# Kernel optimization log

Hardware: AMD Instinct MI355X
Metric: run time of the kernel (lower is better)

The kernel has to match this reference:

```python
import jax, jax.numpy as jnp
import numpy as np

B, L, E, C = 256, 1024, 128, 5  # trees, leaves per tree, embed size, num classes

def setup_inputs() -> dict:
    key = jax.random.key(0)
    k1, k2, k3 = jax.random.split(key, 3)
    leaves = jax.random.normal(k1, (B, L, E), dtype=jnp.float32)
    # Glorot-ish scaling so 10 stacked relu(Linear) levels stay well-conditioned
    W = jax.random.normal(k2, (E, 2 * E), dtype=jnp.float32) * (2.0 / (2 * E)) ** 0.5
    bW = jnp.zeros((E,), dtype=jnp.float32)
    P = jax.random.normal(k3, (C, E), dtype=jnp.float32) * (2.0 / E) ** 0.5
    bP = jnp.zeros((C,), dtype=jnp.float32)
    return {"leaves": leaves, "W": W, "bW": bW, "P": P, "bP": bP}

def reference(leaves, W, bW, P, bP):
    """Batched level-by-level bottom-up pass over a forest of perfect binary trees.
    Per internal node (same math as RecursiveNN.traverse):
        h = relu(W @ concat(left, right) + bW)
        proj = P @ h + bP
    Returns all internal-node projections concatenated: [B*(L-1), C].
    """
    x = leaves  # [B, n, E] current frontier of node embeddings
    probs = []
    while x.shape[1] > 1:
        # pair adjacent siblings: [B, n/2, 2E]
        pairs = jnp.concatenate([x[:, 0::2], x[:, 1::2]], axis=-1)
        h = jax.nn.relu(jnp.einsum('bnf,ef->bne', pairs, W) + bW)  # [B, n/2, E]
        proj = jnp.einsum('bne,ce->bnc', h, P) + bP                # [B, n/2, C]
        probs.append(proj.reshape(-1, P.shape[0]))
        x = h
    return jnp.concatenate(probs, axis=0)  # [B*(L-1), C]
```

## Files before the change

kernel.cpp:

```cpp
#include <hip/hip_runtime.h>
#include <hip/hip_bf16.h>
#include <hip/hip_fp16.h>


typedef _Float16 f16_t;
typedef _Float16 f16x4 __attribute__((ext_vector_type(4)));
typedef _Float16 f16x8 __attribute__((ext_vector_type(8)));
typedef float f32x4 __attribute__((ext_vector_type(4)));

#define HSTRIDE 136

static __device__ __forceinline__ f32x4 mfma16(f16x8 a, f16x8 b, f32x4 c) {
    return __builtin_amdgcn_mfma_f32_16x16x32_f16(a, b, c, 0, 0, 0);
}

static __device__ __forceinline__ f16x8 cvt8(const float* p) {
    const float4 a = *(const float4*)p;
    const float4 b = *(const float4*)(p + 4);
    f16x8 t = { (f16_t)a.x, (f16_t)a.y, (f16_t)a.z, (f16_t)a.w,
                (f16_t)b.x, (f16_t)b.y, (f16_t)b.z, (f16_t)b.w };
    return t;
}

__global__ __launch_bounds__(256, 2)
void forest_kernel(const float* __restrict__ leaves,
                   const float* __restrict__ W,
                   const float* __restrict__ P,
                   const float* __restrict__ bW,
                   const float* __restrict__ bP,
                   f16_t* __restrict__ Q,
                   float* __restrict__ out)
{
    __shared__ f16_t Stg[2][32 * HSTRIDE];
    __shared__ f16_t Hbuf[64 * HSTRIDE];

    const int tid   = threadIdx.x;
    const int wave  = tid >> 6;
    const int lane  = tid & 63;
    const int mlane = lane & 15;
    const int q     = lane >> 4;
    const int tree  = blockIdx.x >> 3;
    const int e     = blockIdx.x & 7;
    const size_t m0 = (size_t)blockIdx.x * 64;
    const float* leafbase = leaves + (size_t)blockIdx.x * 16384;

    auto store_stage = [&](int buf, const float4* pf) {
        #pragma unroll
        for (int r = 0; r < 4; ++r) {
            const int idx = tid + r * 256;
            const int row = idx >> 5;
            const int c4  = idx & 31;
            f16x4 t4 = { (f16_t)pf[r].x, (f16_t)pf[r].y, (f16_t)pf[r].z, (f16_t)pf[r].w };
            *(f16x4*)&Stg[buf][row * HSTRIDE + c4 * 4] = t4;
        }
    };

    float4 pf[4];
    #pragma unroll
    for (int r = 0; r < 4; ++r) pf[r] = ((const float4*)leafbase)[tid + r * 256];

    f16x8 wh[2][8];
    float bwv[2];
    #pragma unroll
    for (int n = 0; n < 2; ++n) {
        const int col = wave * 32 + n * 16 + mlane;
        bwv[n] = bW[col];
        #pragma unroll
        for (int k = 0; k < 8; ++k)
            wh[n][k] = cvt8(&W[col * 256 + k * 32 + q * 8]);
    }

    f16x8 pb[4] = {};
    if (mlane < 5) {
        #pragma unroll
        for (int kb = 0; kb < 4; ++kb)
            pb[kb] = cvt8(&P[mlane * 128 + kb * 32 + q * 8]);
    }
    const float bpv = (mlane < 5) ? bP[mlane] : 0.f;

    store_stage(0, pf);

    auto proj_store = [&](int hrow0, size_t orow0, int valid) {
        f32x4 pc = {};
        #pragma unroll
        for (int kb = 0; kb < 4; ++kb) {
            const f16x8 ha = *(const f16x8*)&Hbuf[(hrow0 + mlane) * HSTRIDE + kb * 32 + q * 8];
            pc = mfma16(ha, pb[kb], pc);
        }
        if (mlane < 5) {
            #pragma unroll
            for (int r = 0; r < 4; ++r) {
                const int row = q * 4 + r;
                if (row < valid) out[(orow0 + row) * 5 + mlane] = pc[r] + bpv;
            }
        }
    };

    for (int c = 0; c < 4; ++c) {
        __syncthreads();
        if (c < 3) {
            #pragma unroll
            for (int r = 0; r < 4; ++r)
                pf[r] = ((const float4*)leafbase)[(c + 1) * 1024 + tid + r * 256];
        }
        f16x8 af[8];
        const f16_t* sb = Stg[c & 1];
        #pragma unroll
        for (int k = 0; k < 8; ++k) {
            const int off  = k * 64 + q * 16;
            const int trow = off >> 8;
            const int ce   = (off & 255) >> 1;
            af[k] = *(const f16x8*)&sb[(2 * mlane + trow) * HSTRIDE + ce];
        }
        f32x4 acc0 = {}, acc1 = {};
        #pragma unroll
        for (int k = 0; k < 8; ++k) {
            acc0 = mfma16(af[k], wh[0][k], acc0);
            acc1 = mfma16(af[k], wh[1][k], acc1);
        }
        if (c < 3) store_stage((c + 1) & 1, pf);

        #pragma unroll
        for (int r = 0; r < 4; ++r) {
            float v0 = fmaxf(acc0[r] + bwv[0], 0.f);
            float v1 = fmaxf(acc1[r] + bwv[1], 0.f);
            Hbuf[(c * 16 + q * 4 + r) * HSTRIDE + wave * 32 + mlane]      = (f16_t)v0;
            Hbuf[(c * 16 + q * 4 + r) * HSTRIDE + wave * 32 + 16 + mlane] = (f16_t)v1;
        }
        __syncthreads();

        if (wave == 0) proj_store(c * 16, m0 + c * 16, 16);
    }

    int Mprev = 64;
    #pragma unroll 1
    for (int j = 2; j <= 7; ++j) {
        const int Mnew   = Mprev >> 1;
        const int chunks = (Mnew + 15) >> 4;
        const size_t off_j = 256 * (1024 - (2048 >> j));
        const size_t base_j = off_j + (size_t)tree * (1024 >> j) + (size_t)e * (128 >> j);
        for (int c = 0; c < chunks; ++c) {
            f16x8 af[8];
            #pragma unroll
            for (int k = 0; k < 8; ++k) {
                const int off  = k * 64 + q * 16;
                const int trow = off >> 8;
                const int ce   = (off & 255) >> 1;
                af[k] = *(const f16x8*)&Hbuf[(32 * c + 2 * mlane + trow) * HSTRIDE + ce];
            }
            __syncthreads();
            f32x4 acc0 = {}, acc1 = {};
            #pragma unroll
            for (int k = 0; k < 8; ++k) {
                acc0 = mfma16(af[k], wh[0][k], acc0);
                acc1 = mfma16(af[k], wh[1][k], acc1);
            }
            #pragma unroll
            for (int r = 0; r < 4; ++r) {
                float v0 = fmaxf(acc0[r] + bwv[0], 0.f);
                float v1 = fmaxf(acc1[r] + bwv[1], 0.f);
                Hbuf[(c * 16 + q * 4 + r) * HSTRIDE + wave * 32 + mlane]      = (f16_t)v0;
                Hbuf[(c * 16 + q * 4 + r) * HSTRIDE + wave * 32 + 16 + mlane] = (f16_t)v1;
            }
            __syncthreads();

            const int valid = (Mnew - c * 16 < 16) ? (Mnew - c * 16) : 16;
            if (wave == 0)
                proj_store(c * 16, base_j + c * 16, valid);
        }
        Mprev = Mnew;
    }

    if (tid < 16)
        *(uint4*)&Q[(size_t)blockIdx.x * 128 + tid * 8] = *(const uint4*)&Hbuf[tid * 8];
}

__global__ __launch_bounds__(128, 4)
void rnn_top_kernel(const f16_t* __restrict__ Q,
                    const float* __restrict__ W,
                    const float* __restrict__ bW,
                    const float* __restrict__ P,
                    const float* __restrict__ bP,
                    float* __restrict__ out)
{
    __shared__ float qs[1024];
    __shared__ float hs[896];
    const int t    = threadIdx.x;
    const int tree = blockIdx.x;

    #pragma unroll
    for (int i = 0; i < 8; ++i)
        qs[t + i * 128] = (float)Q[(size_t)tree * 1024 + t + i * 128];
    __syncthreads();

    const float* wr = W + t * 256;

    float s8[4];
    #pragma unroll
    for (int n = 0; n < 4; ++n) s8[n] = bW[t];
    for (int k = 0; k < 256; k += 4) {
        const float4 wv = *(const float4*)(wr + k);
        #pragma unroll
        for (int n = 0; n < 4; ++n) {
            const float* qb = qs + n * 256 + k;
            s8[n] += wv.x * qb[0] + wv.y * qb[1] + wv.z * qb[2] + wv.w * qb[3];
        }
    }
    #pragma unroll
    for (int n = 0; n < 4; ++n) hs[n * 128 + t] = fmaxf(s8[n], 0.f);
    __syncthreads();

    float s9[2];
    s9[0] = s9[1] = bW[t];
    for (int k = 0; k < 256; k += 4) {
        const float4 wv = *(const float4*)(wr + k);
        #pragma unroll
        for (int m = 0; m < 2; ++m) {
            const float* hb = hs + m * 256 + k;
            s9[m] += wv.x * hb[0] + wv.y * hb[1] + wv.z * hb[2] + wv.w * hb[3];
        }
    }
    hs[512 + t] = fmaxf(s9[0], 0.f);
    hs[640 + t] = fmaxf(s9[1], 0.f);
    __syncthreads();

    float s10 = bW[t];
    for (int k = 0; k < 256; k += 4) {
        const float4 wv = *(const float4*)(wr + k);
        const float* hb = hs + 512 + k;
        s10 += wv.x * hb[0] + wv.y * hb[1] + wv.z * hb[2] + wv.w * hb[3];
    }
    hs[768 + t] = fmaxf(s10, 0.f);
    __syncthreads();

    if (t < 35) {
        const int node = t / 5, c = t % 5;
        float s = bP[c];
        const float* hb = hs + node * 128;
        for (int k = 0; k < 128; ++k) s += hb[k] * P[c * 128 + k];
        size_t row;
        if (node < 4)      row = 260096 + (size_t)tree * 4 + node;
        else if (node < 6) row = 261120 + (size_t)tree * 2 + (node - 4);
        else               row = 261632 + (size_t)tree;
        out[row * 5 + c] = s;
    }
}

extern "C" void kernel_launch(void* const* d_in, const int* in_sizes, int n_in,
                              void* d_out, int out_size, void* d_ws, size_t ws_size,
                              hipStream_t stream) {
    const float* leaves = (const float*)d_in[0];
    const float* W      = (const float*)d_in[1];
    const float* bW     = (const float*)d_in[2];
    const float* P      = (const float*)d_in[3];
    const float* bP     = (const float*)d_in[4];
    float* out = (float*)d_out;

    f16_t* Q = (f16_t*)d_ws;

    forest_kernel<<<dim3(2048), dim3(256), 0, stream>>>(leaves, W, P, bW, bP, Q, out);
    rnn_top_kernel<<<dim3(256), dim3(128), 0, stream>>>(Q, W, bW, P, bP, out);
}
```

Baseline: 248.0 us.

## Preconvert weights to fp16, bulk-load leaves, and stage upper-level outputs in LDS

A new prep kernel converts W and P to fp16 once, so each forest block loads half-precision weights directly instead of converting fp32 on every block. The double-buffered leaf pipeline is replaced by one bulk load of all 64 leaf rows into a larger LDS arena. The level-1 projection is now spread across all four waves after a single barrier. Projections for levels 2-7 are buffered in shared memory and written out cooperatively at the end, rather than as scattered small stores from a single wave. In exchange there is an extra kernel launch and more LDS per block, which may reduce occupancy, and the load/compute overlap of the old pipeline is lost.

```diff
diff --git a/kernel.cpp b/kernel.cpp
--- a/kernel.cpp
+++ b/kernel.cpp
@@ -14,25 +14,28 @@
     return __builtin_amdgcn_mfma_f32_16x16x32_f16(a, b, c, 0, 0, 0);
 }
 
-static __device__ __forceinline__ f16x8 cvt8(const float* p) {
-    const float4 a = *(const float4*)p;
-    const float4 b = *(const float4*)(p + 4);
-    f16x8 t = { (f16_t)a.x, (f16_t)a.y, (f16_t)a.z, (f16_t)a.w,
-                (f16_t)b.x, (f16_t)b.y, (f16_t)b.z, (f16_t)b.w };
-    return t;
+__global__ void prep_kernel(const float* __restrict__ W, const float* __restrict__ P,
+                            f16_t* __restrict__ Wh, f16_t* __restrict__ Ph) {
+    if (blockIdx.x < 128) {
+        const int i = blockIdx.x * 256 + threadIdx.x;
+        Wh[i] = (f16_t)W[i];
+    } else {
+        for (int i = threadIdx.x; i < 640; i += 256) Ph[i] = (f16_t)P[i];
+    }
 }
 
 __global__ __launch_bounds__(256, 2)
 void forest_kernel(const float* __restrict__ leaves,
-                   const float* __restrict__ W,
-                   const float* __restrict__ P,
+                   const f16_t* __restrict__ Wh,
+                   const f16_t* __restrict__ Ph,
                    const float* __restrict__ bW,
                    const float* __restrict__ bP,
                    f16_t* __restrict__ Q,
                    float* __restrict__ out)
 {
-    __shared__ f16_t Stg[2][32 * HSTRIDE];
+    __shared__ f16_t Arena[128 * HSTRIDE];
     __shared__ f16_t Hbuf[64 * HSTRIDE];
+    __shared__ float OutB[320];
 
     const int tid   = threadIdx.x;
     const int wave  = tid >> 6;
@@ -44,21 +47,6 @@
     const size_t m0 = (size_t)blockIdx.x * 64;
     const float* leafbase = leaves + (size_t)blockIdx.x * 16384;
 
-    auto store_stage = [&](int buf, const float4* pf) {
-        #pragma unroll
-        for (int r = 0; r < 4; ++r) {
-            const int idx = tid + r * 256;
-            const int row = idx >> 5;
-            const int c4  = idx & 31;
-            f16x4 t4 = { (f16_t)pf[r].x, (f16_t)pf[r].y, (f16_t)pf[r].z, (f16_t)pf[r].w };
-            *(f16x4*)&Stg[buf][row * HSTRIDE + c4 * 4] = t4;
-        }
-    };
-
-    float4 pf[4];
-    #pragma unroll
-    for (int r = 0; r < 4; ++r) pf[r] = ((const float4*)leafbase)[tid + r * 256];
-
     f16x8 wh[2][8];
     float bwv[2];
     #pragma unroll
@@ -67,50 +55,43 @@
         bwv[n] = bW[col];
         #pragma unroll
         for (int k = 0; k < 8; ++k)
-            wh[n][k] = cvt8(&W[col * 256 + k * 32 + q * 8]);
+            wh[n][k] = *(const f16x8*)&Wh[col * 256 + k * 32 + q * 8];
     }
 
     f16x8 pb[4] = {};
     if (mlane < 5) {
         #pragma unroll
         for (int kb = 0; kb < 4; ++kb)
-            pb[kb] = cvt8(&P[mlane * 128 + kb * 32 + q * 8]);
+            pb[kb] = *(const f16x8*)&Ph[mlane * 128 + kb * 32 + q * 8];
     }
     const float bpv = (mlane < 5) ? bP[mlane] : 0.f;
 
-    store_stage(0, pf);
-
-    auto proj_store = [&](int hrow0, size_t orow0, int valid) {
-        f32x4 pc = {};
-        #pragma unroll
-        for (int kb = 0; kb < 4; ++kb) {
-            const f16x8 ha = *(const f16x8*)&Hbuf[(hrow0 + mlane) * HSTRIDE + kb * 32 + q * 8];
-            pc = mfma16(ha, pb[kb], pc);
-        }
-        if (mlane < 5) {
-            #pragma unroll
-            for (int r = 0; r < 4; ++r) {
-                const int row = q * 4 + r;
-                if (row < valid) out[(orow0 + row) * 5 + mlane] = pc[r] + bpv;
-            }
-        }
-    };
-
+    #pragma unroll
+    for (int b = 0; b < 2; ++b) {
+        float4 t[8];
+        #pragma unroll
+        for (int r = 0; r < 8; ++r)
+            t[r] = ((const float4*)leafbase)[tid + (b * 8 + r) * 256];
+        #pragma unroll
+        for (int r = 0; r < 8; ++r) {
+            const int idx = tid + (b * 8 + r) * 256;
+            const int row = idx >> 5;
+            const int c4  = idx & 31;
+            f16x4 t4 = { (f16_t)t[r].x, (f16_t)t[r].y, (f16_t)t[r].z, (f16_t)t[r].w };
+            *(f16x4*)&Arena[row * HSTRIDE + c4 * 4] = t4;
+        }
+    }
+    __syncthreads();
+
+    #pragma unroll
     for (int c = 0; c < 4; ++c) {
-        __syncthreads();
-        if (c < 3) {
-            #pragma unroll
-            for (int r = 0; r < 4; ++r)
-                pf[r] = ((const float4*)leafbase)[(c + 1) * 1024 + tid + r * 256];
-        }
         f16x8 af[8];
-        const f16_t* sb = Stg[c & 1];
         #pragma unroll
         for (int k = 0; k < 8; ++k) {
             const int off  = k * 64 + q * 16;
             const int trow = off >> 8;
             const int ce   = (off & 255) >> 1;
-            af[k] = *(const f16x8*)&sb[(2 * mlane + trow) * HSTRIDE + ce];
+            af[k] = *(const f16x8*)&Arena[(32 * c + 2 * mlane + trow) * HSTRIDE + ce];
         }
         f32x4 acc0 = {}, acc1 = {};
         #pragma unroll
@@ -118,8 +99,6 @@
             acc0 = mfma16(af[k], wh[0][k], acc0);
             acc1 = mfma16(af[k], wh[1][k], acc1);
         }
-        if (c < 3) store_stage((c + 1) & 1, pf);
-
         #pragma unroll
         for (int r = 0; r < 4; ++r) {
             float v0 = fmaxf(acc0[r] + bwv[0], 0.f);
@@ -127,9 +106,24 @@
             Hbuf[(c * 16 + q * 4 + r) * HSTRIDE + wave * 32 + mlane]      = (f16_t)v0;
             Hbuf[(c * 16 + q * 4 + r) * HSTRIDE + wave * 32 + 16 + mlane] = (f16_t)v1;
         }
-        __syncthreads();
-
-        if (wave == 0) proj_store(c * 16, m0 + c * 16, 16);
+    }
+    __syncthreads();
+
+    {
+        const int hrow0 = wave * 16;
+        f32x4 pc = {};
+        #pragma unroll
+        for (int kb = 0; kb < 4; ++kb) {
+            const f16x8 ha = *(const f16x8*)&Hbuf[(hrow0 + mlane) * HSTRIDE + kb * 32 + q * 8];
+            pc = mfma16(ha, pb[kb], pc);
+        }
+        if (mlane < 5) {
+            #pragma unroll
+            for (int r = 0; r < 4; ++r) {
+                const int row = q * 4 + r;
+                out[(m0 + hrow0 + row) * 5 + mlane] = pc[r] + bpv;
+            }
+        }
     }
 
     int Mprev = 64;
@@ -137,8 +131,7 @@
     for (int j = 2; j <= 7; ++j) {
         const int Mnew   = Mprev >> 1;
         const int chunks = (Mnew + 15) >> 4;
-        const size_t off_j = 256 * (1024 - (2048 >> j));
-        const size_t base_j = off_j + (size_t)tree * (1024 >> j) + (size_t)e * (128 >> j);
+        const int obase  = 64 - (256 >> j);
         for (int c = 0; c < chunks; ++c) {
             f16x8 af[8];
             #pragma unroll
@@ -165,10 +158,40 @@
             __syncthreads();
 
             const int valid = (Mnew - c * 16 < 16) ? (Mnew - c * 16) : 16;
-            if (wave == 0)
-                proj_store(c * 16, base_j + c * 16, valid);
+            if (wave == 0) {
+                f32x4 pc = {};
+                #pragma unroll
+                for (int kb = 0; kb < 4; ++kb) {
+                    const f16x8 ha = *(const f16x8*)&Hbuf[(c * 16 + mlane) * HSTRIDE + kb * 32 + q * 8];
+                    pc = mfma16(ha, pb[kb], pc);
+                }
+                if (mlane < 5) {
+                    #pragma unroll
+                    for (int r = 0; r < 4; ++r) {
+                        const int row = q * 4 + r;
+                        if (row < valid)
+                            OutB[(obase + c * 16 + row) * 5 + mlane] = pc[r] + bpv;
+                    }
+                }
+            }
         }
         Mprev = Mnew;
+    }
+    __syncthreads();
+
+    for (int t2 = tid; t2 < 315; t2 += 256) {
+        const int lrow = t2 / 5;
+        const int cls  = t2 - lrow * 5;
+        int j, i;
+        if      (lrow < 32) { j = 2; i = lrow;      }
+        else if (lrow < 48) { j = 3; i = lrow - 32; }
+        else if (lrow < 56) { j = 4; i = lrow - 48; }
+        else if (lrow < 60) { j = 5; i = lrow - 56; }
+        else if (lrow < 62) { j = 6; i = lrow - 60; }
+        else                { j = 7; i = 0;         }
+        const size_t grow = (size_t)256 * (1024 - (2048 >> j))
+                          + (size_t)tree * (1024 >> j) + (size_t)e * (128 >> j) + i;
+        out[grow * 5 + cls] = OutB[t2];
     }
 
     if (tid < 16)
@@ -256,8 +279,11 @@
     const float* bP     = (const float*)d_in[4];
     float* out = (float*)d_out;
 
-    f16_t* Q = (f16_t*)d_ws;
-
-    forest_kernel<<<dim3(2048), dim3(256), 0, stream>>>(leaves, W, P, bW, bP, Q, out);
+    f16_t* Wh = (f16_t*)d_ws;
+    f16_t* Ph = Wh + 32768;
+    f16_t* Q  = Wh + 32768 + 1024;
+
+    prep_kernel<<<dim3(129), dim3(256), 0, stream>>>(W, P, Wh, Ph);
+    forest_kernel<<<dim3(2048), dim3(256), 0, stream>>>(leaves, Wh, Ph, bW, bP, Q, out);
     rnn_top_kernel<<<dim3(256), dim3(128), 0, stream>>>(Q, W, bW, P, bP, out);
 }
```

Result: faster. 226.6 us (-8.6%).
